# Performance work log

Hardware: AMD Instinct MI355X
Metric: run time of the kernel (lower is better)

## Reference

```python
import jax, jax.numpy as jnp
import numpy as np

N, E, D, L, G = 100000, 800000, 64, 5, 256
ATOM_VOCAB, BOND_VOCAB = 119, 5
BN_EPS = 1e-5

def _bn(h, g, b):
    # BatchNorm1d in training mode: batch mean / biased var over nodes
    m = h.mean(0)
    v = h.var(0)
    return g * (h - m) * jax.lax.rsqrt(v + BN_EPS) + b

def setup_inputs() -> dict:
    key = jax.random.key(0)
    ks = jax.random.split(key, 12)
    xavier = lambda k, fi, fo: jax.random.uniform(k, (fi, fo), jnp.float32,
                                                  -np.sqrt(6.0/(fi+fo)), np.sqrt(6.0/(fi+fo)))
    return {
        "batch": jnp.sort(jax.random.randint(ks[0], (N,), 0, G)),
        "x": jax.random.randint(ks[1], (N, 1), 0, ATOM_VOCAB),
        "edge_index": jax.random.randint(ks[2], (2, E), 0, N),
        "edge_attr": jax.random.randint(ks[3], (E, 1), 0, BOND_VOCAB),
        "atom_emb": jax.random.normal(ks[4], (ATOM_VOCAB, D), jnp.float32),
        "bond_emb": jax.random.normal(ks[5], (BOND_VOCAB, D), jnp.float32),
        "W1": jnp.stack([xavier(jax.random.fold_in(ks[6], i), D, 2*D) for i in range(L)]),
        "b1": jnp.zeros((L, 2*D), jnp.float32),
        "g1": jnp.ones((L, 2*D), jnp.float32),
        "be1": jnp.zeros((L, 2*D), jnp.float32),
        "W2": jnp.stack([xavier(jax.random.fold_in(ks[7], i), 2*D, D) for i in range(L)]),
        "b2": jnp.zeros((L, D), jnp.float32),
        "gbn": jnp.ones((L, D), jnp.float32),
        "bbn": jnp.zeros((L, D), jnp.float32),
    }

def reference(batch, x, edge_index, edge_attr, atom_emb, bond_emb,
              W1, b1, g1, be1, W2, b2, gbn, bbn):
    h = atom_emb[x[:, 0]]              # [N, D]
    ea = bond_emb[edge_attr[:, 0]]     # [E, D]
    src, dst = edge_index[0], edge_index[1]
    for i in range(L):
        msg = jax.nn.relu(h[src] + ea)                         # [E, D]
        aggr = jax.ops.segment_sum(msg, dst, num_segments=N)   # [N, D]
        z = h + aggr                                           # (1+eps)*x_i + aggr, eps=0
        z = _bn(z @ W1[i] + b1[i], g1[i], be1[i])
        z = jax.nn.relu(z) @ W2[i] + b2[i]
        h = _bn(z, gbn[i], bbn[i])                             # outer BN
        if i < L - 1:
            h = jax.nn.relu(h)                                 # drop_ratio = 0 -> no dropout
    xpool = jax.ops.segment_sum(h, batch, num_segments=G)      # global_add_pool
    return (xpool, h)
```

## Files before the change

kernel.cpp:

```cpp
#include <hip/hip_runtime.h>
#include <cstdint>
#include <cstddef>

#define NN 100000
#define NP 100032
#define NE 800000
#define NG 256
#define NL 5
#define EPS 1e-5f
#define NSTRIPE 32

typedef __bf16 bf16x8 __attribute__((ext_vector_type(8)));
typedef float f32x4 __attribute__((ext_vector_type(4)));

__device__ __forceinline__ float bf2f(unsigned short u) {
  union { unsigned int i; float f; } x; x.i = ((unsigned int)u) << 16; return x.f;
}
__device__ __forceinline__ unsigned short f2bf(float f) {
  union { float f; unsigned int i; } x; x.f = f;
  unsigned int r = x.i + 0x7fffu + ((x.i >> 16) & 1u);
  return (unsigned short)(r >> 16);
}

__global__ __launch_bounds__(256) void prep_k(const int* __restrict__ x,
                                              const float* __restrict__ atom_emb,
                                              unsigned short* __restrict__ A,
                                              const float* __restrict__ W1,
                                              const float* __restrict__ W2,
                                              unsigned short* __restrict__ Wt1,
                                              unsigned short* __restrict__ Wt2,
                                              int* __restrict__ cnt) {
  int b = blockIdx.x, t = threadIdx.x;
  if (b < 3125) {
    int i = b * 256 + t;
    int n = i >> 3, c0 = (i & 7) * 8;
    const float* p = atom_emb + (size_t)x[n] * 64 + c0;
    float4 v0 = *(const float4*)p;
    float4 v1 = *(const float4*)(p + 4);
    union { bf16x8 b8; unsigned short u[8]; } o;
    o.u[0] = f2bf(v0.x); o.u[1] = f2bf(v0.y); o.u[2] = f2bf(v0.z); o.u[3] = f2bf(v0.w);
    o.u[4] = f2bf(v1.x); o.u[5] = f2bf(v1.y); o.u[6] = f2bf(v1.z); o.u[7] = f2bf(v1.w);
    *(bf16x8*)(A + (size_t)n * 64 + c0) = o.b8;
  } else if (b < 3445) {
    int i = (b - 3125) * 256 + t;
    const int S = NL * 128 * 64;
    if (i < S) {
      int l = i / (128 * 64), r = i % (128 * 64);
      int c = r / 64, k = r % 64;
      Wt1[i] = f2bf(W1[(size_t)l * 64 * 128 + (size_t)k * 128 + c]);
    } else {
      int j = i - S;
      int l = j / (128 * 64), r = j % (128 * 64);
      int c = r / 128, k = r % 128;
      Wt2[j] = f2bf(W2[(size_t)l * 128 * 64 + (size_t)k * 64 + c]);
    }
  } else {
    int i = (b - 3445) * 256 + t;
    if (i < NN) cnt[i] = 0;
  }
}

__global__ __launch_bounds__(256) void hist_k(const int* __restrict__ ei,
                                              int* __restrict__ cnt) {
  int e = blockIdx.x * 256 + threadIdx.x;
  if (e >= NE) return;
  atomicAdd(&cnt[ei[NE + e]], 1);
}

__global__ __launch_bounds__(256) void scan1_k(const int* __restrict__ cnt,
                                               int* __restrict__ rs,
                                               int* __restrict__ bsum) {
  __shared__ int sh[256];
  int t = threadIdx.x;
  int base = blockIdx.x * 1024 + t * 4;
  int v0 = 0, v1 = 0, v2 = 0, v3 = 0;
  if (base + 0 < NN) v0 = cnt[base + 0];
  if (base + 1 < NN) v1 = cnt[base + 1];
  if (base + 2 < NN) v2 = cnt[base + 2];
  if (base + 3 < NN) v3 = cnt[base + 3];
  int tsum = v0 + v1 + v2 + v3;
  sh[t] = tsum;
  __syncthreads();
  for (int off = 1; off < 256; off <<= 1) {
    int x = (t >= off) ? sh[t - off] : 0;
    __syncthreads();
    sh[t] += x;
    __syncthreads();
  }
  int excl = sh[t] - tsum;
  if (base + 0 < NN) rs[base + 0] = excl;
  if (base + 1 < NN) rs[base + 1] = excl + v0;
  if (base + 2 < NN) rs[base + 2] = excl + v0 + v1;
  if (base + 3 < NN) rs[base + 3] = excl + v0 + v1 + v2;
  if (t == 255) bsum[blockIdx.x] = sh[255];
}

__global__ __launch_bounds__(256) void scan3_k(int* __restrict__ rs,
                                               const int* __restrict__ bsum,
                                               int* __restrict__ cursor) {
  int i = blockIdx.x * 256 + threadIdx.x;
  int chunk = blockIdx.x >> 2;
  int boff = 0;
  for (int j = 0; j < chunk; ++j) boff += bsum[j];
  if (i < NN) {
    int v = rs[i] + boff;
    rs[i] = v;
    cursor[i] = v;
  }
  if (i == 0) rs[NN] = NE;
}

__global__ __launch_bounds__(256) void scatter_k(const int* __restrict__ ei,
                                                 const int* __restrict__ eattr,
                                                 int* __restrict__ cursor,
                                                 int* __restrict__ epack) {
  int band = blockIdx.x & 3;
  int e = (blockIdx.x >> 2) * 256 + threadIdx.x;
  if (e >= NE) return;
  int d = ei[NE + e];
  if (d / 25000 != band) return;
  int slot = atomicAdd(&cursor[d], 1);
  epack[slot] = (ei[e] << 3) | eattr[e];
}

template <int MODE>
__global__ __launch_bounds__(256) void csr_aggr_k(const int* __restrict__ rowstart,
                                                  const int* __restrict__ epack,
                                                  const float* __restrict__ bond,
                                                  const unsigned short* __restrict__ A,
                                                  const float* __restrict__ stat2prev,
                                                  const float* __restrict__ g,
                                                  const float* __restrict__ be,
                                                  const unsigned short* __restrict__ Wt1,
                                                  unsigned short* __restrict__ B,
                                                  float* __restrict__ stat1) {
  __shared__ float bl[5][68];
  __shared__ float scl64[64], shf64[64];
  __shared__ unsigned short Bs[32][72];
  int tid = threadIdx.x;
  for (int j = tid; j < 320; j += 256) bl[j >> 6][j & 63] = bond[j];
  if (MODE && tid < 64) {
    float s = 0.f, s2 = 0.f;
#pragma unroll
    for (int r = 0; r < NSTRIPE; ++r) {
      s += stat2prev[r * 128 + tid];
      s2 += stat2prev[r * 128 + 64 + tid];
    }
    float mean = s * (1.f / NN);
    float var = fmaxf(s2 * (1.f / NN) - mean * mean, 0.f);
    float sc = g[tid] * rsqrtf(var + EPS);
    scl64[tid] = sc;
    shf64[tid] = be[tid] - mean * sc;
  }
  __syncthreads();

  int lane = tid & 63;
  int sg = lane >> 3, ch = lane & 7, c0 = ch * 8;
  int rloc = (tid >> 6) * 8 + sg;
  int row = blockIdx.x * 32 + rloc;
  float sc[8], sf[8];
  if (MODE) {
#pragma unroll
    for (int j = 0; j < 8; ++j) { sc[j] = scl64[c0 + j]; sf[j] = shf64[c0 + j]; }
  }
  int s = rowstart[row], e = rowstart[row + 1];
  float acc[8];
#pragma unroll
  for (int j = 0; j < 8; ++j) acc[j] = 0.f;
  int i = s;
  for (; i + 2 <= e; i += 2) {
    int p0 = epack[i], p1 = epack[i + 1];
    union { bf16x8 b; unsigned short u[8]; } h0, h1;
    h0.b = *(const bf16x8*)(A + (size_t)(p0 >> 3) * 64 + c0);
    h1.b = *(const bf16x8*)(A + (size_t)(p1 >> 3) * 64 + c0);
    const float* bp0 = &bl[p0 & 7][c0];
    const float* bp1 = &bl[p1 & 7][c0];
    float4 a0 = *(const float4*)(bp0), a1 = *(const float4*)(bp0 + 4);
    float4 d0 = *(const float4*)(bp1), d1 = *(const float4*)(bp1 + 4);
    float bb0[8] = {a0.x, a0.y, a0.z, a0.w, a1.x, a1.y, a1.z, a1.w};
    float bb1[8] = {d0.x, d0.y, d0.z, d0.w, d1.x, d1.y, d1.z, d1.w};
#pragma unroll
    for (int j = 0; j < 8; ++j) {
      float v0 = bf2f(h0.u[j]);
      float v1 = bf2f(h1.u[j]);
      if (MODE) {
        v0 = fmaxf(fmaf(v0, sc[j], sf[j]), 0.f);
        v1 = fmaxf(fmaf(v1, sc[j], sf[j]), 0.f);
      }
      acc[j] += fmaxf(v0 + bb0[j], 0.f);
      acc[j] += fmaxf(v1 + bb1[j], 0.f);
    }
  }
  if (i < e) {
    int p0 = epack[i];
    union { bf16x8 b; unsigned short u[8]; } h0;
    h0.b = *(const bf16x8*)(A + (size_t)(p0 >> 3) * 64 + c0);
    const float* bp0 = &bl[p0 & 7][c0];
    float4 a0 = *(const float4*)(bp0), a1 = *(const float4*)(bp0 + 4);
    float bb0[8] = {a0.x, a0.y, a0.z, a0.w, a1.x, a1.y, a1.z, a1.w};
#pragma unroll
    for (int j = 0; j < 8; ++j) {
      float v0 = bf2f(h0.u[j]);
      if (MODE) v0 = fmaxf(fmaf(v0, sc[j], sf[j]), 0.f);
      acc[j] += fmaxf(v0 + bb0[j], 0.f);
    }
  }
  union { bf16x8 b; unsigned short u[8]; } rv, o;
  rv.b = *(const bf16x8*)(A + (size_t)row * 64 + c0);
#pragma unroll
  for (int j = 0; j < 8; ++j) {
    float r = bf2f(rv.u[j]);
    if (MODE) r = fmaxf(fmaf(r, sc[j], sf[j]), 0.f);
    o.u[j] = f2bf(acc[j] + r);
  }
  *(bf16x8*)(B + (size_t)row * 64 + c0) = o.b;
  *(bf16x8*)&Bs[rloc][c0] = o.b;
  __syncthreads();

  int w = tid >> 6;
  int rlo = lane & 15, khi = lane >> 4;
  int tile = w >> 1, gcol = (w & 1) * 64;
  bf16x8 fa0 = *(const bf16x8*)&Bs[tile * 16 + rlo][khi * 8];
  bf16x8 fa1 = *(const bf16x8*)&Bs[tile * 16 + rlo][khi * 8 + 32];
  float* dst = stat1 + (blockIdx.x & (NSTRIPE - 1)) * 256;
#pragma unroll
  for (int ct = 0; ct < 4; ++ct) {
    int c = gcol + ct * 16 + rlo;
    const bf16x8* bp = (const bf16x8*)(Wt1 + (size_t)c * 64 + khi * 8);
    f32x4 yacc;
    yacc[0] = 0.f; yacc[1] = 0.f; yacc[2] = 0.f; yacc[3] = 0.f;
    yacc = __builtin_amdgcn_mfma_f32_16x16x32_bf16(fa0, bp[0], yacc, 0, 0, 0);
    yacc = __builtin_amdgcn_mfma_f32_16x16x32_bf16(fa1, bp[4], yacc, 0, 0, 0);
    float ss = 0.f, ss2 = 0.f;
#pragma unroll
    for (int q = 0; q < 4; ++q) {
      ss += yacc[q];
      ss2 = fmaf(yacc[q], yacc[q], ss2);
    }
    ss += __shfl_xor(ss, 16);  ss += __shfl_xor(ss, 32);
    ss2 += __shfl_xor(ss2, 16); ss2 += __shfl_xor(ss2, 32);
    if (khi == 0) {
      atomicAdd(&dst[c], ss);
      atomicAdd(&dst[128 + c], ss2);
    }
  }
}

__global__ __launch_bounds__(256) void gemm12_k(const unsigned short* __restrict__ B,
                                                const unsigned short* __restrict__ Wt1,
                                                const unsigned short* __restrict__ Wt2,
                                                const float* __restrict__ stat1,
                                                const float* __restrict__ g1,
                                                const float* __restrict__ be1,
                                                const float* __restrict__ b2,
                                                unsigned short* __restrict__ z2b,
                                                float* __restrict__ stat2f) {
  __shared__ unsigned short Zs[64][136];
  __shared__ float sclS[128], shfS[128], sred[128];
  int tid = threadIdx.x;
  int w = tid >> 6, lane = tid & 63;
  int rlo = lane & 15, khi = lane >> 4;
  int row0 = blockIdx.x * 64 + w * 16;
  const bf16x8* ap = (const bf16x8*)(B + (size_t)(row0 + rlo) * 64 + khi * 8);
  bf16x8 a0 = ap[0], a1 = ap[4];
  if (tid < 128) {
    float s = 0.f, s2 = 0.f;
#pragma unroll
    for (int r = 0; r < NSTRIPE; ++r) {
      s += stat1[r * 256 + tid];
      s2 += stat1[r * 256 + 128 + tid];
    }
    float mean = s * (1.f / NN);
    float var = fmaxf(s2 * (1.f / NN) - mean * mean, 0.f);
    float sc = g1[tid] * rsqrtf(var + EPS);
    sclS[tid] = sc;
    shfS[tid] = be1[tid] - mean * sc;
    sred[tid] = 0.f;
  }
  __syncthreads();
#pragma unroll
  for (int ct = 0; ct < 8; ++ct) {
    const bf16x8* bp = (const bf16x8*)(Wt1 + (size_t)(ct * 16 + rlo) * 64 + khi * 8);
    f32x4 acc;
    acc[0] = 0.f; acc[1] = 0.f; acc[2] = 0.f; acc[3] = 0.f;
    acc = __builtin_amdgcn_mfma_f32_16x16x32_bf16(a0, bp[0], acc, 0, 0, 0);
    acc = __builtin_amdgcn_mfma_f32_16x16x32_bf16(a1, bp[4], acc, 0, 0, 0);
    int c = ct * 16 + rlo;
    float sc = sclS[c], sf = shfS[c];
#pragma unroll
    for (int q = 0; q < 4; ++q)
      Zs[w * 16 + khi * 4 + q][c] = f2bf(fmaxf(fmaf(acc[q], sc, sf), 0.f));
  }
  bf16x8 af0 = *(const bf16x8*)&Zs[w * 16 + rlo][khi * 8];
  bf16x8 af1 = *(const bf16x8*)&Zs[w * 16 + rlo][32 + khi * 8];
  bf16x8 af2 = *(const bf16x8*)&Zs[w * 16 + rlo][64 + khi * 8];
  bf16x8 af3 = *(const bf16x8*)&Zs[w * 16 + rlo][96 + khi * 8];
  __syncthreads();
  f32x4 acc2[4];
#pragma unroll
  for (int ct = 0; ct < 4; ++ct) { acc2[ct][0] = 0.f; acc2[ct][1] = 0.f; acc2[ct][2] = 0.f; acc2[ct][3] = 0.f; }
#pragma unroll
  for (int ct = 0; ct < 4; ++ct) {
    const bf16x8* bp = (const bf16x8*)(Wt2 + (size_t)(ct * 16 + rlo) * 128 + khi * 8);
    acc2[ct] = __builtin_amdgcn_mfma_f32_16x16x32_bf16(af0, bp[0], acc2[ct], 0, 0, 0);
    acc2[ct] = __builtin_amdgcn_mfma_f32_16x16x32_bf16(af1, bp[4], acc2[ct], 0, 0, 0);
    acc2[ct] = __builtin_amdgcn_mfma_f32_16x16x32_bf16(af2, bp[8], acc2[ct], 0, 0, 0);
    acc2[ct] = __builtin_amdgcn_mfma_f32_16x16x32_bf16(af3, bp[12], acc2[ct], 0, 0, 0);
  }
  unsigned short (*Z2)[72] = (unsigned short(*)[72])Zs;
#pragma unroll
  for (int ct = 0; ct < 4; ++ct) {
    int c = ct * 16 + rlo;
    float bs = b2[c];
    float s = 0.f, s2 = 0.f;
#pragma unroll
    for (int q = 0; q < 4; ++q) {
      int brow = w * 16 + khi * 4 + q;
      float v = acc2[ct][q] + bs;
      unsigned short ub = f2bf(v);
      Z2[brow][c] = ub;
      float vf = bf2f(ub);
      if (blockIdx.x * 64 + brow < NN) { s += vf; s2 += vf * vf; }
    }
    s += __shfl_xor(s, 16);  s += __shfl_xor(s, 32);
    s2 += __shfl_xor(s2, 16); s2 += __shfl_xor(s2, 32);
    if (khi == 0) {
      atomicAdd(&sred[c], s);
      atomicAdd(&sred[64 + c], s2);
    }
  }
  __syncthreads();
#pragma unroll
  for (int pass = 0; pass < 2; ++pass) {
    int orow = pass * 32 + (tid >> 3), oc0 = (tid & 7) * 8;
    *(bf16x8*)(z2b + (size_t)(blockIdx.x * 64 + orow) * 64 + oc0) =
        *(const bf16x8*)&Z2[orow][oc0];
  }
  if (tid < 128)
    atomicAdd(&stat2f[(blockIdx.x & (NSTRIPE - 1)) * 128 + tid], sred[tid]);
}

__global__ __launch_bounds__(256) void final_k(const unsigned short* __restrict__ A,
                                               const float* __restrict__ stat2f,
                                               const float* __restrict__ g,
                                               const float* __restrict__ be,
                                               const int* __restrict__ batch,
                                               float* __restrict__ hf,
                                               float* __restrict__ xpool) {
  __shared__ float scl[64], shf[64];
  __shared__ float red[16][64];
  __shared__ int gfirst, gsame;
  int tid = threadIdx.x;
  if (tid < 64) {
    float s = 0.f, s2 = 0.f;
#pragma unroll
    for (int r = 0; r < NSTRIPE; ++r) {
      s += stat2f[r * 128 + tid];
      s2 += stat2f[r * 128 + 64 + tid];
    }
    float mean = s * (1.f / NN);
    float var = fmaxf(s2 * (1.f / NN) - mean * mean, 0.f);
    float sc = g[tid] * rsqrtf(var + EPS);
    scl[tid] = sc;
    shf[tid] = be[tid] - mean * sc;
  }
  int n0 = blockIdx.x * 16;
  if (tid == 0) {
    gfirst = batch[n0];
    gsame = (batch[n0] == batch[n0 + 15]) ? 1 : 0;
  }
  __syncthreads();
  int r = tid >> 4, c4 = tid & 15;
  int n = n0 + r;
  ushort4 raw = *(const ushort4*)(A + (size_t)n * 64 + c4 * 4);
  int cb = c4 * 4;
  float4 v;
  v.x = fmaf(bf2f(raw.x), scl[cb + 0], shf[cb + 0]);
  v.y = fmaf(bf2f(raw.y), scl[cb + 1], shf[cb + 1]);
  v.z = fmaf(bf2f(raw.z), scl[cb + 2], shf[cb + 2]);
  v.w = fmaf(bf2f(raw.w), scl[cb + 3], shf[cb + 3]);
  *(float4*)(hf + (size_t)n * 64 + cb) = v;
  *(float4*)&red[r][cb] = v;
  __syncthreads();
  if (gsame) {
#pragma unroll
    for (int off = 8; off >= 1; off >>= 1) {
      if (r < off) {
        float4 a = *(float4*)&red[r][cb];
        float4 b = *(float4*)&red[r + off][cb];
        *(float4*)&red[r][cb] = make_float4(a.x + b.x, a.y + b.y, a.z + b.z, a.w + b.w);
      }
      __syncthreads();
    }
    if (r == 0) {
      float* p = xpool + (size_t)gfirst * 64 + cb;
      float4 a = *(float4*)&red[0][cb];
      atomicAdd(p + 0, a.x); atomicAdd(p + 1, a.y);
      atomicAdd(p + 2, a.z); atomicAdd(p + 3, a.w);
    }
  } else {
    int gg = batch[n];
    float* p = xpool + (size_t)gg * 64 + cb;
    atomicAdd(p + 0, v.x); atomicAdd(p + 1, v.y);
    atomicAdd(p + 2, v.z); atomicAdd(p + 3, v.w);
  }
}

extern "C" void kernel_launch(void* const* d_in, const int* in_sizes, int n_in,
                              void* d_out, int out_size, void* d_ws, size_t ws_size,
                              hipStream_t stream) {
  const int* batch = (const int*)d_in[0];
  const int* x = (const int*)d_in[1];
  const int* ei = (const int*)d_in[2];
  const int* eattr = (const int*)d_in[3];
  const float* atom_emb = (const float*)d_in[4];
  const float* bond_emb = (const float*)d_in[5];
  const float* W1 = (const float*)d_in[6];
  const float* g1 = (const float*)d_in[8];
  const float* be1 = (const float*)d_in[9];
  const float* W2 = (const float*)d_in[10];
  const float* b2 = (const float*)d_in[11];
  const float* gbn = (const float*)d_in[12];
  const float* bbn = (const float*)d_in[13];

  float* out = (float*)d_out;
  float* xpool = out;
  float* hf = out + NG * 64;

  char* ws = (char*)d_ws;
  unsigned short* A   = (unsigned short*)(ws);
  unsigned short* B   = (unsigned short*)(ws + 12804096);
  float* sbuf         = (float*)(ws + 25608192);
  unsigned short* Wt1 = (unsigned short*)(ws + 25853952);
  unsigned short* Wt2 = (unsigned short*)(ws + 25935872);
  int* rowstart       = (int*)(ws + 26017792);
  int* epack          = (int*)(ws + 26417796);
  int* cnt    = (int*)(ws + 12804096);
  int* cursor = (int*)(ws + 12804096 + 1048576);
  int* bsum   = (int*)(ws + 12804096 + 2097152);

  prep_k<<<3836, 256, 0, stream>>>(x, atom_emb, A, W1, W2, Wt1, Wt2, cnt);

  hist_k<<<(NE + 255) / 256, 256, 0, stream>>>(ei, cnt);
  scan1_k<<<98, 256, 0, stream>>>(cnt, rowstart, bsum);
  scan3_k<<<(NN + 255) / 256, 256, 0, stream>>>(rowstart, bsum, cursor);
  scatter_k<<<4 * ((NE + 255) / 256), 256, 0, stream>>>(ei, eattr, cursor, epack);

  hipMemsetAsync(sbuf, 0, 245760, stream);
  for (int l = 0; l < NL; ++l) {
    float* stat1 = sbuf + (size_t)l * 12288;
    float* stat2 = sbuf + (size_t)l * 12288 + 8192;
    float* stat2p = sbuf + (size_t)(l - 1) * 12288 + 8192;
    if (l == 0)
      csr_aggr_k<0><<<NN / 32, 256, 0, stream>>>(rowstart, epack, bond_emb, A,
                                                 sbuf, gbn, bbn,
                                                 Wt1, B, stat1);
    else
      csr_aggr_k<1><<<NN / 32, 256, 0, stream>>>(rowstart, epack, bond_emb, A,
                                                 stat2p, gbn + (size_t)(l - 1) * 64,
                                                 bbn + (size_t)(l - 1) * 64,
                                                 Wt1 + (size_t)l * 128 * 64, B, stat1);
    gemm12_k<<<NP / 64, 256, 0, stream>>>(B, Wt1 + (size_t)l * 128 * 64,
                                          Wt2 + (size_t)l * 64 * 128,
                                          stat1, g1 + (size_t)l * 128, be1 + (size_t)l * 128,
                                          b2 + (size_t)l * 64, A, stat2);
  }

  hipMemsetAsync(xpool, 0, (size_t)NG * 64 * 4, stream);
  final_k<<<NN / 16, 256, 0, stream>>>(A, sbuf + (size_t)(NL - 1) * 12288 + 8192,
                                       gbn + (size_t)(NL - 1) * 64,
                                       bbn + (size_t)(NL - 1) * 64, batch, hf, xpool);
}
```

Measured before the change: 484.8 us.

## Batch CSR edge index loads via shuffles and double rows per GEMM block

The CSR aggregation loop now fetches up to eight edge indices at once with one coalesced load per lane group and broadcasts them with shuffles. It then issues up to eight independent row gathers before accumulating, which raises memory-level parallelism over the old two-at-a-time loop. The fused GEMM kernel now processes two 64-row tiles per block, halving the grid and amortising the per-block BN-stat reduction and atomics. The padded row count and workspace offsets change to match. The cost is more registers in the aggregation kernel and an extra sync per tile in the GEMM.

Measured after the change: 503.1 us. 3.8% more time.

```diff
diff --git a/kernel.cpp b/kernel.cpp
--- a/kernel.cpp
+++ b/kernel.cpp
@@ -3,7 +3,7 @@
 #include <cstddef>
 
 #define NN 100000
-#define NP 100032
+#define NP 100096
 #define NE 800000
 #define NG 256
 #define NL 5
@@ -167,42 +167,30 @@
   float acc[8];
 #pragma unroll
   for (int j = 0; j < 8; ++j) acc[j] = 0.f;
-  int i = s;
-  for (; i + 2 <= e; i += 2) {
-    int p0 = epack[i], p1 = epack[i + 1];
-    union { bf16x8 b; unsigned short u[8]; } h0, h1;
-    h0.b = *(const bf16x8*)(A + (size_t)(p0 >> 3) * 64 + c0);
-    h1.b = *(const bf16x8*)(A + (size_t)(p1 >> 3) * 64 + c0);
-    const float* bp0 = &bl[p0 & 7][c0];
-    const float* bp1 = &bl[p1 & 7][c0];
-    float4 a0 = *(const float4*)(bp0), a1 = *(const float4*)(bp0 + 4);
-    float4 d0 = *(const float4*)(bp1), d1 = *(const float4*)(bp1 + 4);
-    float bb0[8] = {a0.x, a0.y, a0.z, a0.w, a1.x, a1.y, a1.z, a1.w};
-    float bb1[8] = {d0.x, d0.y, d0.z, d0.w, d1.x, d1.y, d1.z, d1.w};
+  for (int base = s; base < e; base += 8) {
+    int m = e - base; if (m > 8) m = 8;
+    int pk = (ch < m) ? epack[base + ch] : 0;
+    int p[8];
+#pragma unroll
+    for (int j = 0; j < 8; ++j) p[j] = __shfl(pk, sg * 8 + j);
+    union { bf16x8 b; unsigned short u[8]; } hv[8];
+#pragma unroll
+    for (int j = 0; j < 8; ++j)
+      if (j < m) hv[j].b = *(const bf16x8*)(A + (size_t)(p[j] >> 3) * 64 + c0);
 #pragma unroll
     for (int j = 0; j < 8; ++j) {
-      float v0 = bf2f(h0.u[j]);
-      float v1 = bf2f(h1.u[j]);
-      if (MODE) {
-        v0 = fmaxf(fmaf(v0, sc[j], sf[j]), 0.f);
-        v1 = fmaxf(fmaf(v1, sc[j], sf[j]), 0.f);
+      if (j < m) {
+        const float* bp = &bl[p[j] & 7][c0];
+        float4 b0 = *(const float4*)(bp);
+        float4 b1 = *(const float4*)(bp + 4);
+        float bb[8] = {b0.x, b0.y, b0.z, b0.w, b1.x, b1.y, b1.z, b1.w};
+#pragma unroll
+        for (int q = 0; q < 8; ++q) {
+          float v = bf2f(hv[j].u[q]);
+          if (MODE) v = fmaxf(fmaf(v, sc[q], sf[q]), 0.f);
+          acc[q] += fmaxf(v + bb[q], 0.f);
+        }
       }
-      acc[j] += fmaxf(v0 + bb0[j], 0.f);
-      acc[j] += fmaxf(v1 + bb1[j], 0.f);
-    }
-  }
-  if (i < e) {
-    int p0 = epack[i];
-    union { bf16x8 b; unsigned short u[8]; } h0;
-    h0.b = *(const bf16x8*)(A + (size_t)(p0 >> 3) * 64 + c0);
-    const float* bp0 = &bl[p0 & 7][c0];
-    float4 a0 = *(const float4*)(bp0), a1 = *(const float4*)(bp0 + 4);
-    float bb0[8] = {a0.x, a0.y, a0.z, a0.w, a1.x, a1.y, a1.z, a1.w};
-#pragma unroll
-    for (int j = 0; j < 8; ++j) {
-      float v0 = bf2f(h0.u[j]);
-      if (MODE) v0 = fmaxf(fmaf(v0, sc[j], sf[j]), 0.f);
-      acc[j] += fmaxf(v0 + bb0[j], 0.f);
     }
   }
   union { bf16x8 b; unsigned short u[8]; } rv, o;
@@ -260,9 +248,9 @@
   int tid = threadIdx.x;
   int w = tid >> 6, lane = tid & 63;
   int rlo = lane & 15, khi = lane >> 4;
-  int row0 = blockIdx.x * 64 + w * 16;
-  const bf16x8* ap = (const bf16x8*)(B + (size_t)(row0 + rlo) * 64 + khi * 8);
-  bf16x8 a0 = ap[0], a1 = ap[4];
+  int rowbase = blockIdx.x * 128;
+  const bf16x8* ap0 = (const bf16x8*)(B + (size_t)(rowbase + w * 16 + rlo) * 64 + khi * 8);
+  bf16x8 a0 = ap0[0], a1 = ap0[4];
   if (tid < 128) {
     float s = 0.f, s2 = 0.f;
 #pragma unroll
@@ -278,63 +266,73 @@
     sred[tid] = 0.f;
   }
   __syncthreads();
-#pragma unroll
-  for (int ct = 0; ct < 8; ++ct) {
-    const bf16x8* bp = (const bf16x8*)(Wt1 + (size_t)(ct * 16 + rlo) * 64 + khi * 8);
-    f32x4 acc;
-    acc[0] = 0.f; acc[1] = 0.f; acc[2] = 0.f; acc[3] = 0.f;
-    acc = __builtin_amdgcn_mfma_f32_16x16x32_bf16(a0, bp[0], acc, 0, 0, 0);
-    acc = __builtin_amdgcn_mfma_f32_16x16x32_bf16(a1, bp[4], acc, 0, 0, 0);
-    int c = ct * 16 + rlo;
-    float sc = sclS[c], sf = shfS[c];
-#pragma unroll
-    for (int q = 0; q < 4; ++q)
-      Zs[w * 16 + khi * 4 + q][c] = f2bf(fmaxf(fmaf(acc[q], sc, sf), 0.f));
-  }
-  bf16x8 af0 = *(const bf16x8*)&Zs[w * 16 + rlo][khi * 8];
-  bf16x8 af1 = *(const bf16x8*)&Zs[w * 16 + rlo][32 + khi * 8];
-  bf16x8 af2 = *(const bf16x8*)&Zs[w * 16 + rlo][64 + khi * 8];
-  bf16x8 af3 = *(const bf16x8*)&Zs[w * 16 + rlo][96 + khi * 8];
-  __syncthreads();
-  f32x4 acc2[4];
-#pragma unroll
-  for (int ct = 0; ct < 4; ++ct) { acc2[ct][0] = 0.f; acc2[ct][1] = 0.f; acc2[ct][2] = 0.f; acc2[ct][3] = 0.f; }
-#pragma unroll
-  for (int ct = 0; ct < 4; ++ct) {
-    const bf16x8* bp = (const bf16x8*)(Wt2 + (size_t)(ct * 16 + rlo) * 128 + khi * 8);
-    acc2[ct] = __builtin_amdgcn_mfma_f32_16x16x32_bf16(af0, bp[0], acc2[ct], 0, 0, 0);
-    acc2[ct] = __builtin_amdgcn_mfma_f32_16x16x32_bf16(af1, bp[4], acc2[ct], 0, 0, 0);
-    acc2[ct] = __builtin_amdgcn_mfma_f32_16x16x32_bf16(af2, bp[8], acc2[ct], 0, 0, 0);
-    acc2[ct] = __builtin_amdgcn_mfma_f32_16x16x32_bf16(af3, bp[12], acc2[ct], 0, 0, 0);
-  }
-  unsigned short (*Z2)[72] = (unsigned short(*)[72])Zs;
-#pragma unroll
-  for (int ct = 0; ct < 4; ++ct) {
-    int c = ct * 16 + rlo;
-    float bs = b2[c];
-    float s = 0.f, s2 = 0.f;
-#pragma unroll
-    for (int q = 0; q < 4; ++q) {
-      int brow = w * 16 + khi * 4 + q;
-      float v = acc2[ct][q] + bs;
-      unsigned short ub = f2bf(v);
-      Z2[brow][c] = ub;
-      float vf = bf2f(ub);
-      if (blockIdx.x * 64 + brow < NN) { s += vf; s2 += vf * vf; }
-    }
-    s += __shfl_xor(s, 16);  s += __shfl_xor(s, 32);
-    s2 += __shfl_xor(s2, 16); s2 += __shfl_xor(s2, 32);
-    if (khi == 0) {
-      atomicAdd(&sred[c], s);
-      atomicAdd(&sred[64 + c], s2);
-    }
-  }
-  __syncthreads();
-#pragma unroll
-  for (int pass = 0; pass < 2; ++pass) {
-    int orow = pass * 32 + (tid >> 3), oc0 = (tid & 7) * 8;
-    *(bf16x8*)(z2b + (size_t)(blockIdx.x * 64 + orow) * 64 + oc0) =
-        *(const bf16x8*)&Z2[orow][oc0];
+
+#pragma unroll
+  for (int t = 0; t < 2; ++t) {
+    int row0 = rowbase + t * 64 + w * 16;
+    if (t == 1) {
+      const bf16x8* ap = (const bf16x8*)(B + (size_t)(row0 + rlo) * 64 + khi * 8);
+      a0 = ap[0]; a1 = ap[4];
+    }
+#pragma unroll
+    for (int ct = 0; ct < 8; ++ct) {
+      const bf16x8* bp = (const bf16x8*)(Wt1 + (size_t)(ct * 16 + rlo) * 64 + khi * 8);
+      f32x4 acc;
+      acc[0] = 0.f; acc[1] = 0.f; acc[2] = 0.f; acc[3] = 0.f;
+      acc = __builtin_amdgcn_mfma_f32_16x16x32_bf16(a0, bp[0], acc, 0, 0, 0);
+      acc = __builtin_amdgcn_mfma_f32_16x16x32_bf16(a1, bp[4], acc, 0, 0, 0);
+      int c = ct * 16 + rlo;
+      float sc = sclS[c], sf = shfS[c];
+#pragma unroll
+      for (int q = 0; q < 4; ++q)
+        Zs[w * 16 + khi * 4 + q][c] = f2bf(fmaxf(fmaf(acc[q], sc, sf), 0.f));
+    }
+    bf16x8 af0 = *(const bf16x8*)&Zs[w * 16 + rlo][khi * 8];
+    bf16x8 af1 = *(const bf16x8*)&Zs[w * 16 + rlo][32 + khi * 8];
+    bf16x8 af2 = *(const bf16x8*)&Zs[w * 16 + rlo][64 + khi * 8];
+    bf16x8 af3 = *(const bf16x8*)&Zs[w * 16 + rlo][96 + khi * 8];
+    __syncthreads();
+    f32x4 acc2[4];
+#pragma unroll
+    for (int ct = 0; ct < 4; ++ct) { acc2[ct][0] = 0.f; acc2[ct][1] = 0.f; acc2[ct][2] = 0.f; acc2[ct][3] = 0.f; }
+#pragma unroll
+    for (int ct = 0; ct < 4; ++ct) {
+      const bf16x8* bp = (const bf16x8*)(Wt2 + (size_t)(ct * 16 + rlo) * 128 + khi * 8);
+      acc2[ct] = __builtin_amdgcn_mfma_f32_16x16x32_bf16(af0, bp[0], acc2[ct], 0, 0, 0);
+      acc2[ct] = __builtin_amdgcn_mfma_f32_16x16x32_bf16(af1, bp[4], acc2[ct], 0, 0, 0);
+      acc2[ct] = __builtin_amdgcn_mfma_f32_16x16x32_bf16(af2, bp[8], acc2[ct], 0, 0, 0);
+      acc2[ct] = __builtin_amdgcn_mfma_f32_16x16x32_bf16(af3, bp[12], acc2[ct], 0, 0, 0);
+    }
+    unsigned short (*Z2)[72] = (unsigned short(*)[72])Zs;
+#pragma unroll
+    for (int ct = 0; ct < 4; ++ct) {
+      int c = ct * 16 + rlo;
+      float bs = b2[c];
+      float s = 0.f, s2 = 0.f;
+#pragma unroll
+      for (int q = 0; q < 4; ++q) {
+        int grow = row0 + khi * 4 + q;
+        float v = acc2[ct][q] + bs;
+        unsigned short ub = f2bf(v);
+        Z2[w * 16 + khi * 4 + q][c] = ub;
+        float vf = bf2f(ub);
+        if (grow < NN) { s += vf; s2 += vf * vf; }
+      }
+      s += __shfl_xor(s, 16);  s += __shfl_xor(s, 32);
+      s2 += __shfl_xor(s2, 16); s2 += __shfl_xor(s2, 32);
+      if (khi == 0) {
+        atomicAdd(&sred[c], s);
+        atomicAdd(&sred[64 + c], s2);
+      }
+    }
+    __syncthreads();
+#pragma unroll
+    for (int pass = 0; pass < 2; ++pass) {
+      int orow = pass * 32 + (tid >> 3), oc0 = (tid & 7) * 8;
+      *(bf16x8*)(z2b + (size_t)(rowbase + t * 64 + orow) * 64 + oc0) =
+          *(const bf16x8*)&Z2[orow][oc0];
+    }
+    __syncthreads();
   }
   if (tid < 128)
     atomicAdd(&stat2f[(blockIdx.x & (NSTRIPE - 1)) * 128 + tid], sred[tid]);
@@ -429,15 +427,15 @@
 
   char* ws = (char*)d_ws;
   unsigned short* A   = (unsigned short*)(ws);
-  unsigned short* B   = (unsigned short*)(ws + 12804096);
-  float* sbuf         = (float*)(ws + 25608192);
-  unsigned short* Wt1 = (unsigned short*)(ws + 25853952);
-  unsigned short* Wt2 = (unsigned short*)(ws + 25935872);
-  int* rowstart       = (int*)(ws + 26017792);
-  int* epack          = (int*)(ws + 26417796);
-  int* cnt    = (int*)(ws + 12804096);
-  int* cursor = (int*)(ws + 12804096 + 1048576);
-  int* bsum   = (int*)(ws + 12804096 + 2097152);
+  unsigned short* B   = (unsigned short*)(ws + 12812288);
+  float* sbuf         = (float*)(ws + 25624576);
+  unsigned short* Wt1 = (unsigned short*)(ws + 25870336);
+  unsigned short* Wt2 = (unsigned short*)(ws + 25952256);
+  int* rowstart       = (int*)(ws + 26034176);
+  int* epack          = (int*)(ws + 26434304);
+  int* cnt    = (int*)(ws + 12812288);
+  int* cursor = (int*)(ws + 12812288 + 1048576);
+  int* bsum   = (int*)(ws + 12812288 + 2097152);
 
   prep_k<<<3836, 256, 0, stream>>>(x, atom_emb, A, W1, W2, Wt1, Wt2, cnt);
 
@@ -460,10 +458,10 @@
                                                  stat2p, gbn + (size_t)(l - 1) * 64,
                                                  bbn + (size_t)(l - 1) * 64,
                                                  Wt1 + (size_t)l * 128 * 64, B, stat1);
-    gemm12_k<<<NP / 64, 256, 0, stream>>>(B, Wt1 + (size_t)l * 128 * 64,
-                                          Wt2 + (size_t)l * 64 * 128,
-                                          stat1, g1 + (size_t)l * 128, be1 + (size_t)l * 128,
-                                          b2 + (size_t)l * 64, A, stat2);
+    gemm12_k<<<NP / 128, 256, 0, stream>>>(B, Wt1 + (size_t)l * 128 * 64,
+                                           Wt2 + (size_t)l * 64 * 128,
+                                           stat1, g1 + (size_t)l * 128, be1 + (size_t)l * 128,
+                                           b2 + (size_t)l * 64, A, stat2);
   }
 
   hipMemsetAsync(xpool, 0, (size_t)NG * 64 * 4, stream);
```
